# Kernel tuning notes

Hardware: AMD Instinct MI355X
Metric: run time of the kernel (lower is better)

## Reference

```python
import jax, jax.numpy as jnp
import numpy as np

EPS = 1e-6

def absmean_quantize(W):
    # gamma = mean |W| + eps; quantize to {-1,0,1}
    gamma = jnp.abs(W).mean() + EPS
    Ws = W / gamma
    return jnp.sign(Ws) * jnp.minimum(jnp.round(jnp.abs(Ws)), 1.0)

def setup_inputs() -> dict:
    key = jax.random.key(0)
    k1, k2 = jax.random.split(key)
    B, S, D_IN, D_OUT = 4, 2048, 4096, 16384
    x = jax.random.normal(k1, (B, S, D_IN), dtype=jnp.float32)
    weight = jax.random.normal(k2, (D_OUT, D_IN), dtype=jnp.float32)
    return {"x": x, "weight": weight}

def reference(x, weight):
    # BitLinear158 forward: ternary-quantize weight, then linear (no bias)
    qw = absmean_quantize(weight)  # [out, in]
    return jnp.einsum('bsi,oi->bso', x, qw)
```

## Files before the change

### kernel.cpp

```cpp
#include <hip/hip_runtime.h>
#include <stdint.h>

typedef int i32x4 __attribute__((ext_vector_type(4)));

#define M_DIM 8192
#define N_DIM 16384
#define K_DIM 4096

#define BM 128
#define BN 128
#define BK 64

__device__ __forceinline__ void gload_lds16(const void* g, void* l) {
  __builtin_amdgcn_global_load_lds((const __attribute__((address_space(1))) void*)g,
                                   (__attribute__((address_space(3))) void*)l,
                                   16, 0, 0);
}

__global__ __launch_bounds__(256) void reduce_kernel(const float* __restrict__ W,
                                                     const float* __restrict__ x,
                                                     double* __restrict__ gsum,
                                                     unsigned* __restrict__ xmax,
                                                     int nW4, int nX4) {
  int tid = blockIdx.x * blockDim.x + threadIdx.x;
  int stride = gridDim.x * blockDim.x;
  const float4* W4 = (const float4*)W;
  const float4* X4 = (const float4*)x;
  double s = 0.0;
  for (int i = tid; i < nW4; i += stride) {
    float4 v = W4[i];
    s += (double)fabsf(v.x) + (double)fabsf(v.y) +
         (double)fabsf(v.z) + (double)fabsf(v.w);
  }
  float m = 0.f;
  for (int i = tid; i < nX4; i += stride) {
    float4 v = X4[i];
    m = fmaxf(m, fmaxf(fmaxf(fabsf(v.x), fabsf(v.y)), fmaxf(fabsf(v.z), fabsf(v.w))));
  }
  for (int off = 32; off > 0; off >>= 1) {
    s += __shfl_down(s, off, 64);
    m = fmaxf(m, __shfl_down(m, off, 64));
  }
  __shared__ double wsum[4];
  __shared__ float wmax[4];
  int l = threadIdx.x & 63, w = threadIdx.x >> 6;
  if (l == 0) { wsum[w] = s; wmax[w] = m; }
  __syncthreads();
  if (threadIdx.x == 0) {
    atomicAdd(gsum, wsum[0] + wsum[1] + wsum[2] + wsum[3]);
    float mm = fmaxf(fmaxf(wmax[0], wmax[1]), fmaxf(wmax[2], wmax[3]));
    atomicMax(xmax, __float_as_uint(mm));
  }
}

__global__ __launch_bounds__(256) void quant_kernel(const float* __restrict__ W,
                                                    const double* __restrict__ gsum,
                                                    char* __restrict__ Bq, int n4) {
  float gamma = (float)(*gsum * (1.0 / (double)((size_t)N_DIM * K_DIM))) + 1e-6f;
  int tid = blockIdx.x * blockDim.x + threadIdx.x;
  int stride = gridDim.x * blockDim.x;
  const float4* W4 = (const float4*)W;
  char4* B4 = (char4*)Bq;
  for (int i = tid; i < n4; i += stride) {
    float4 v = W4[i];
    float q0 = copysignf(fminf(rintf(fabsf(v.x / gamma)), 1.0f), v.x);
    float q1 = copysignf(fminf(rintf(fabsf(v.y / gamma)), 1.0f), v.y);
    float q2 = copysignf(fminf(rintf(fabsf(v.z / gamma)), 1.0f), v.z);
    float q3 = copysignf(fminf(rintf(fabsf(v.w / gamma)), 1.0f), v.w);
    char4 o;
    o.x = (char)(int)q0; o.y = (char)(int)q1;
    o.z = (char)(int)q2; o.w = (char)(int)q3;
    B4[i] = o;
  }
}

__global__ __launch_bounds__(256) void split_kernel(const float* __restrict__ x,
                                                    const unsigned* __restrict__ xmax,
                                                    char* __restrict__ hi,
                                                    char* __restrict__ lo, int n4) {
  float amax = __uint_as_float(*xmax);
  float inv = 32512.f / (amax + 1e-30f);
  int tid = blockIdx.x * blockDim.x + threadIdx.x;
  int stride = gridDim.x * blockDim.x;
  const float4* X4 = (const float4*)x;
  char4* H4 = (char4*)hi;
  char4* L4 = (char4*)lo;
  for (int i = tid; i < n4; i += stride) {
    float4 v = X4[i];
    float q[4] = {v.x, v.y, v.z, v.w};
    char hh[4], ll[4];
#pragma unroll
    for (int j = 0; j < 4; ++j) {
      float qf = fminf(fmaxf(rintf(q[j] * inv), -32512.f), 32512.f);
      float hf = rintf(qf * (1.f / 256.f));
      float lf = qf - 256.f * hf;
      if (lf > 127.f) { hf += 1.f; lf -= 256.f; }
      hh[j] = (char)(int)hf;
      ll[j] = (char)(int)lf;
    }
    char4 h = {hh[0], hh[1], hh[2], hh[3]};
    char4 l = {ll[0], ll[1], ll[2], ll[3]};
    H4[i] = h;
    L4[i] = l;
  }
}

__global__ __launch_bounds__(512, 4) void gemm_kernel(const char* __restrict__ Ahi,
                                                      const char* __restrict__ Alo,
                                                      const char* __restrict__ Bq,
                                                      const unsigned* __restrict__ xmax,
                                                      float* __restrict__ C) {
  __shared__ __align__(16) char lds[24576];

  int wg = blockIdx.x;
  wg = (wg & 7) * 1024 + (wg >> 3);
  const int tm = wg >> 7;
  const int tn = wg & 127;

  const int tid = threadIdx.x;
  const int w = tid >> 6;
  const int l = tid & 63;
  const int wr = w >> 2;
  const int wc = w & 3;
  const int lr15 = l & 15;
  const int lk16 = (l >> 4) << 4;

  const char* srcs[3];
  const char* dsts[3];
#pragma unroll
  for (int j = 0; j < 3; ++j) {
    int job = w * 3 + j;
    const char* base = (job < 8) ? Ahi : (job < 16) ? Alo : Bq;
    int s = job & 7;
    int rowb = (job < 16) ? tm * BM : tn * BN;
    srcs[j] = base + (size_t)(rowb + s * 16 + lr15) * K_DIM + lk16;
    dsts[j] = &lds[job * 1024];
  }

  i32x4 acch[4][2], accl[4][2];
#pragma unroll
  for (int m = 0; m < 4; ++m)
#pragma unroll
    for (int n = 0; n < 2; ++n) {
      acch[m][n] = (i32x4){0, 0, 0, 0};
      accl[m][n] = (i32x4){0, 0, 0, 0};
    }

  for (int k0 = 0; k0 < K_DIM; k0 += BK) {
#pragma unroll
    for (int j = 0; j < 3; ++j)
      gload_lds16(srcs[j] + k0, (void*)(dsts[j]));
    __syncthreads();

    i32x4 b0 = *(const i32x4*)&lds[16384 + (wc * 2 + 0) * 1024 + l * 16];
    i32x4 b1 = *(const i32x4*)&lds[16384 + (wc * 2 + 1) * 1024 + l * 16];
#pragma unroll
    for (int m = 0; m < 4; ++m) {
      i32x4 a = *(const i32x4*)&lds[(wr * 4 + m) * 1024 + l * 16];
      acch[m][0] = __builtin_amdgcn_mfma_i32_16x16x64_i8(a, b0, acch[m][0], 0, 0, 0);
      acch[m][1] = __builtin_amdgcn_mfma_i32_16x16x64_i8(a, b1, acch[m][1], 0, 0, 0);
    }
#pragma unroll
    for (int m = 0; m < 4; ++m) {
      i32x4 a = *(const i32x4*)&lds[8192 + (wr * 4 + m) * 1024 + l * 16];
      accl[m][0] = __builtin_amdgcn_mfma_i32_16x16x64_i8(a, b0, accl[m][0], 0, 0, 0);
      accl[m][1] = __builtin_amdgcn_mfma_i32_16x16x64_i8(a, b1, accl[m][1], 0, 0, 0);
    }
    __syncthreads();
  }

  const float sc = __uint_as_float(*xmax) * (1.f / 32512.f);
#pragma unroll
  for (int m = 0; m < 4; ++m) {
    int row = tm * BM + wr * 64 + m * 16 + (l >> 4) * 4;
#pragma unroll
    for (int n = 0; n < 2; ++n) {
      int col = tn * BN + wc * 32 + n * 16 + lr15;
      float* cp = C + (size_t)row * N_DIM + col;
#pragma unroll
      for (int j = 0; j < 4; ++j)
        cp[(size_t)j * N_DIM] = sc * fmaf(256.f, (float)acch[m][n][j], (float)accl[m][n][j]);
    }
  }
}

extern "C" void kernel_launch(void* const* d_in, const int* in_sizes, int n_in,
                              void* d_out, int out_size, void* d_ws, size_t ws_size,
                              hipStream_t stream) {
  const float* x = (const float*)d_in[0];
  const float* W = (const float*)d_in[1];
  float* C = (float*)d_out;

  double* gsum = (double*)d_ws;
  unsigned* xmax = (unsigned*)((char*)d_ws + 8);
  char* Ahi = (char*)d_ws + 256;
  char* Alo = Ahi + (size_t)M_DIM * K_DIM;
  char* Bq  = Alo + (size_t)M_DIM * K_DIM;

  hipMemsetAsync(d_ws, 0, 16, stream);
  reduce_kernel<<<dim3(2048), dim3(256), 0, stream>>>(W, x, gsum, xmax,
                                                      (N_DIM * K_DIM) / 4,
                                                      (M_DIM * K_DIM) / 4);
  quant_kernel<<<dim3(2048), dim3(256), 0, stream>>>(W, gsum, Bq, (N_DIM * K_DIM) / 4);
  split_kernel<<<dim3(2048), dim3(256), 0, stream>>>(x, xmax, Ahi, Alo, (M_DIM * K_DIM) / 4);
  gemm_kernel<<<dim3((M_DIM / BM) * (N_DIM / BN)), dim3(512), 0, stream>>>(Ahi, Alo, Bq, xmax, C);
}
```

Baseline: 2.300 ms.

## Double-buffer GEMM LDS tiles and merge quantize/split prep kernels

```diff
diff --git a/kernel.cpp b/kernel.cpp
--- a/kernel.cpp
+++ b/kernel.cpp
@@ -53,15 +53,25 @@
   }
 }
 
-__global__ __launch_bounds__(256) void quant_kernel(const float* __restrict__ W,
-                                                    const double* __restrict__ gsum,
-                                                    char* __restrict__ Bq, int n4) {
+__global__ __launch_bounds__(256) void prep_kernel(const float* __restrict__ W,
+                                                   const float* __restrict__ x,
+                                                   const double* __restrict__ gsum,
+                                                   const unsigned* __restrict__ xmax,
+                                                   char* __restrict__ Bq,
+                                                   char* __restrict__ hi,
+                                                   char* __restrict__ lo,
+                                                   int nW4, int nX4) {
   float gamma = (float)(*gsum * (1.0 / (double)((size_t)N_DIM * K_DIM))) + 1e-6f;
+  float amax = __uint_as_float(*xmax);
+  float inv = 32512.f / (amax + 1e-30f);
   int tid = blockIdx.x * blockDim.x + threadIdx.x;
   int stride = gridDim.x * blockDim.x;
   const float4* W4 = (const float4*)W;
+  const float4* X4 = (const float4*)x;
   char4* B4 = (char4*)Bq;
-  for (int i = tid; i < n4; i += stride) {
+  char4* H4 = (char4*)hi;
+  char4* L4 = (char4*)lo;
+  for (int i = tid; i < nW4; i += stride) {
     float4 v = W4[i];
     float q0 = copysignf(fminf(rintf(fabsf(v.x / gamma)), 1.0f), v.x);
     float q1 = copysignf(fminf(rintf(fabsf(v.y / gamma)), 1.0f), v.y);
@@ -72,20 +82,7 @@
     o.z = (char)(int)q2; o.w = (char)(int)q3;
     B4[i] = o;
   }
-}
-
-__global__ __launch_bounds__(256) void split_kernel(const float* __restrict__ x,
-                                                    const unsigned* __restrict__ xmax,
-                                                    char* __restrict__ hi,
-                                                    char* __restrict__ lo, int n4) {
-  float amax = __uint_as_float(*xmax);
-  float inv = 32512.f / (amax + 1e-30f);
-  int tid = blockIdx.x * blockDim.x + threadIdx.x;
-  int stride = gridDim.x * blockDim.x;
-  const float4* X4 = (const float4*)x;
-  char4* H4 = (char4*)hi;
-  char4* L4 = (char4*)lo;
-  for (int i = tid; i < n4; i += stride) {
+  for (int i = tid; i < nX4; i += stride) {
     float4 v = X4[i];
     float q[4] = {v.x, v.y, v.z, v.w};
     char hh[4], ll[4];
@@ -105,12 +102,12 @@
   }
 }
 
-__global__ __launch_bounds__(512, 4) void gemm_kernel(const char* __restrict__ Ahi,
+__global__ __launch_bounds__(512, 6) void gemm_kernel(const char* __restrict__ Ahi,
                                                       const char* __restrict__ Alo,
                                                       const char* __restrict__ Bq,
                                                       const unsigned* __restrict__ xmax,
                                                       float* __restrict__ C) {
-  __shared__ __align__(16) char lds[24576];
+  __shared__ __align__(16) char lds[49152];
 
   int wg = blockIdx.x;
   wg = (wg & 7) * 1024 + (wg >> 3);
@@ -126,15 +123,15 @@
   const int lk16 = (l >> 4) << 4;
 
   const char* srcs[3];
-  const char* dsts[3];
+  int jobs[3];
 #pragma unroll
   for (int j = 0; j < 3; ++j) {
     int job = w * 3 + j;
+    jobs[j] = job;
     const char* base = (job < 8) ? Ahi : (job < 16) ? Alo : Bq;
     int s = job & 7;
     int rowb = (job < 16) ? tm * BM : tn * BN;
     srcs[j] = base + (size_t)(rowb + s * 16 + lr15) * K_DIM + lk16;
-    dsts[j] = &lds[job * 1024];
   }
 
   i32x4 acch[4][2], accl[4][2];
@@ -146,27 +143,41 @@
       accl[m][n] = (i32x4){0, 0, 0, 0};
     }
 
-  for (int k0 = 0; k0 < K_DIM; k0 += BK) {
-#pragma unroll
-    for (int j = 0; j < 3; ++j)
-      gload_lds16(srcs[j] + k0, (void*)(dsts[j]));
-    __syncthreads();
-
-    i32x4 b0 = *(const i32x4*)&lds[16384 + (wc * 2 + 0) * 1024 + l * 16];
-    i32x4 b1 = *(const i32x4*)&lds[16384 + (wc * 2 + 1) * 1024 + l * 16];
+#pragma unroll
+  for (int j = 0; j < 3; ++j)
+    gload_lds16(srcs[j], (void*)&lds[jobs[j] * 1024]);
+  asm volatile("s_waitcnt vmcnt(0)" ::: "memory");
+  __builtin_amdgcn_s_barrier();
+
+  for (int t = 0; t < K_DIM / BK; ++t) {
+    const int cur = (t & 1) * 24576;
+    const int nxt = 24576 - cur;
+    if (t < K_DIM / BK - 1) {
+      const int k0 = (t + 1) * BK;
+#pragma unroll
+      for (int j = 0; j < 3; ++j)
+        gload_lds16(srcs[j] + k0, (void*)&lds[nxt + jobs[j] * 1024]);
+    }
+
+    i32x4 b0 = *(const i32x4*)&lds[cur + 16384 + (wc * 2 + 0) * 1024 + l * 16];
+    i32x4 b1 = *(const i32x4*)&lds[cur + 16384 + (wc * 2 + 1) * 1024 + l * 16];
+    __builtin_amdgcn_s_setprio(1);
 #pragma unroll
     for (int m = 0; m < 4; ++m) {
-      i32x4 a = *(const i32x4*)&lds[(wr * 4 + m) * 1024 + l * 16];
+      i32x4 a = *(const i32x4*)&lds[cur + (wr * 4 + m) * 1024 + l * 16];
       acch[m][0] = __builtin_amdgcn_mfma_i32_16x16x64_i8(a, b0, acch[m][0], 0, 0, 0);
       acch[m][1] = __builtin_amdgcn_mfma_i32_16x16x64_i8(a, b1, acch[m][1], 0, 0, 0);
     }
 #pragma unroll
     for (int m = 0; m < 4; ++m) {
-      i32x4 a = *(const i32x4*)&lds[8192 + (wr * 4 + m) * 1024 + l * 16];
+      i32x4 a = *(const i32x4*)&lds[cur + 8192 + (wr * 4 + m) * 1024 + l * 16];
       accl[m][0] = __builtin_amdgcn_mfma_i32_16x16x64_i8(a, b0, accl[m][0], 0, 0, 0);
       accl[m][1] = __builtin_amdgcn_mfma_i32_16x16x64_i8(a, b1, accl[m][1], 0, 0, 0);
     }
-    __syncthreads();
+    __builtin_amdgcn_s_setprio(0);
+
+    asm volatile("s_waitcnt vmcnt(0)" ::: "memory");
+    __builtin_amdgcn_s_barrier();
   }
 
   const float sc = __uint_as_float(*xmax) * (1.f / 32512.f);
@@ -201,7 +212,8 @@
   reduce_kernel<<<dim3(2048), dim3(256), 0, stream>>>(W, x, gsum, xmax,
                                                       (N_DIM * K_DIM) / 4,
                                                       (M_DIM * K_DIM) / 4);
-  quant_kernel<<<dim3(2048), dim3(256), 0, stream>>>(W, gsum, Bq, (N_DIM * K_DIM) / 4);
-  split_kernel<<<dim3(2048), dim3(256), 0, stream>>>(x, xmax, Ahi, Alo, (M_DIM * K_DIM) / 4);
+  prep_kernel<<<dim3(2048), dim3(256), 0, stream>>>(W, x, gsum, xmax, Bq, Ahi, Alo,
+                                                    (N_DIM * K_DIM) / 4,
+                                                    (M_DIM * K_DIM) / 4);
   gemm_kernel<<<dim3((M_DIM / BM) * (N_DIM / BN)), dim3(512), 0, stream>>>(Ahi, Alo, Bq, xmax, C);
 }
```

Result: slower. 5.462 ms (+137.5%).
